# Kernel tuning notes

Measured on AMD Instinct MI355X. Metric: run time of the kernel, lower is better.

Reference implementation:

```python
import jax, jax.numpy as jnp
import numpy as np

B, T, N, D = 256, 200, 8, 64
MODEL = N * D          # 512
FFN_H = 1024 * N // 4  # 2048
EPS = 1.1920929e-07    # torch.finfo(float32).eps (nn.RMSNorm default eps=None)


def setup_inputs() -> dict:
    key = jax.random.key(0)
    ks = jax.random.split(key, 9)
    def xavier(k, shape):
        fan_in, fan_out = shape[-2], shape[-1]
        lim = float(np.sqrt(6.0 / (fan_in + fan_out)))
        return jax.random.uniform(k, shape, jnp.float32, -lim, lim)
    q = jax.random.normal(ks[0], (B, N, D), jnp.float32)
    seq = jax.random.normal(ks[1], (B, T, MODEL), jnp.float32)
    seq_mask = jax.random.randint(ks[2], (B, T), 0, 2) > 0
    seq_mask = seq_mask.at[:, 0].set(True)  # ensure >=1 valid position per row
    return {
        "q": q,
        "seq": seq,
        "rms_w": jnp.ones((MODEL,), jnp.float32),
        "w1": xavier(ks[3], (MODEL, FFN_H)),
        "w2": xavier(ks[4], (MODEL, FFN_H)),
        "w3": xavier(ks[5], (FFN_H, MODEL)),
        "w_k": xavier(ks[6], (N, D, D)),
        "w_v": xavier(ks[7], (N, D, D)),
        "seq_mask": seq_mask,
    }


def reference(q, seq, rms_w, w1, w2, w3, w_k, w_v, seq_mask):
    # RMSNorm
    sn = seq * jax.lax.rsqrt(jnp.mean(seq * seq, axis=-1, keepdims=True) + EPS) * rms_w
    # SwiGLU FFN + residual (dropout=0 / eval)
    h = (jax.nn.silu(sn @ w1) * (sn @ w2)) @ w3 + seq  # (B,T,N*D)
    hh = h.reshape(B, T, N, D)
    keys = jnp.einsum('btnd,nde->bnte', hh, w_k)    # (B,N,T,D)
    values = jnp.einsum('btnd,nde->bnte', hh, w_v)  # (B,N,T,D)
    scale = D ** (-0.5)
    scores = jnp.einsum('bnd,bntd->bnt', q, keys) * scale  # single-query attention
    scores = jnp.where(seq_mask[:, None, :], scores, -jnp.inf)
    attn = jax.nn.softmax(scores, axis=-1)
    ctx = jnp.einsum('bnt,bntd->bnd', attn, values)
    return ctx + q
```

## Files before the change

### kernel.cpp

```cpp
#include <hip/hip_runtime.h>
#include <hip/hip_fp16.h>
#include <cstdint>
#include <cstddef>

typedef unsigned short u16t;
typedef __bf16 bf16x8 __attribute__((ext_vector_type(8)));
typedef float f32x4 __attribute__((ext_vector_type(4)));
typedef unsigned short u16x8 __attribute__((ext_vector_type(8)));

#define BT_ROWS 51200
#define MODEL 512
#define FFNH 2048

__device__ __forceinline__ float bf2f(u16t u) {
  union { unsigned int i; float f; } v; v.i = ((unsigned int)u) << 16; return v.f;
}
__device__ __forceinline__ u16t f2bf(float f) {
  union { float f; unsigned int i; } v; v.f = f;
  return (u16t)((v.i + 0x7fffu + ((v.i >> 16) & 1u)) >> 16);
}
__device__ __forceinline__ float ldf(const void* p, size_t i, int dt) {
  if (dt == 1) return ((const float*)p)[i];
  u16t u = ((const u16t*)p)[i];
  if (dt == 0) return bf2f(u);
  __half h; *(u16t*)&h = u; return __half2float(h);
}
__device__ __forceinline__ void stf(void* p, size_t i, int dt, float f) {
  if (dt == 1) { ((float*)p)[i] = f; }
  else if (dt == 0) { ((u16t*)p)[i] = f2bf(f); }
  else { __half h = __float2half(f); ((u16t*)p)[i] = *(u16t*)&h; }
}
__device__ __forceinline__ void gl2lds16(const void* g, void* l) {
  __builtin_amdgcn_global_load_lds((const __attribute__((address_space(1))) void*)g,
                                   (__attribute__((address_space(3))) void*)l, 16, 0, 0);
}

__global__ __launch_bounds__(256) void detect_dtype_k(const unsigned int* __restrict__ w1,
                                                      int* __restrict__ cnts) {
  int i = blockIdx.x * 256 + threadIdx.x;
  unsigned int w = w1[i];
  u16t lo = (u16t)(w & 0xffffu), hi = (u16t)(w >> 16);
  float flo = bf2f(lo);
  int a = (!(fabsf(flo) < 0.25f)) ? 1 : 0;
  __half hh; *(u16t*)&hh = hi; float fhi = __half2float(hh);
  int b = (fabsf(fhi) > 0.25f && fabsf(fhi) < 256.f) ? 1 : 0;
  unsigned long long ba = __ballot(a), bb = __ballot(b);
  if ((threadIdx.x & 63) == 0) {
    atomicAdd(&cnts[0], (int)__popcll(ba));
    atomicAdd(&cnts[1], (int)__popcll(bb));
  }
}
__global__ void detect_finalize_k(const int* __restrict__ cnts, int* __restrict__ dflag) {
  if (threadIdx.x == 0)
    dflag[0] = (cnts[0] > 4096) ? 1 : ((cnts[1] < 4096) ? 2 : 0);
}

__global__ __launch_bounds__(256) void detect_mask_k(const unsigned int* __restrict__ msk,
                                                     int* __restrict__ flag) {
  int i = blockIdx.x * 256 + threadIdx.x;
  if (i < 12800) {
    unsigned int v = msk[i];
    if (v > 1u) atomicOr(flag, 1);
  }
}

__global__ __launch_bounds__(256) void rmsnorm_k(const void* __restrict__ seq,
                                                 const void* __restrict__ w,
                                                 const int* __restrict__ dfp,
                                                 u16t* __restrict__ xn) {
  const int dt = dfp[0];
  int row = blockIdx.x * 4 + (threadIdx.x >> 6);
  int lane = threadIdx.x & 63;
  size_t base = (size_t)row * MODEL + lane * 8;
  float x[8]; float ss = 0.f;
  if (dt == 0) {
    u16x8 xv = *(const u16x8*)((const u16t*)seq + base);
#pragma unroll
    for (int j = 0; j < 8; j++) { x[j] = bf2f(xv[j]); ss += x[j] * x[j]; }
  } else if (dt == 1) {
    const f32x4* p = (const f32x4*)((const float*)seq + base);
    f32x4 va = p[0], vb = p[1];
#pragma unroll
    for (int j = 0; j < 4; j++) { x[j] = va[j]; x[4 + j] = vb[j]; }
#pragma unroll
    for (int j = 0; j < 8; j++) ss += x[j] * x[j];
  } else {
#pragma unroll
    for (int j = 0; j < 8; j++) { x[j] = ldf(seq, base + j, dt); ss += x[j] * x[j]; }
  }
#pragma unroll
  for (int o = 32; o; o >>= 1) ss += __shfl_xor(ss, o);
  float rstd = rsqrtf(ss * (1.f / 512.f) + 1.1920929e-07f);
  u16x8 ov;
#pragma unroll
  for (int j = 0; j < 8; j++) ov[j] = f2bf(x[j] * rstd * ldf(w, lane * 8 + j, dt));
  *(u16x8*)(xn + base) = ov;
}

__global__ __launch_bounds__(256) void transpose_k(const void* __restrict__ src,
                                                   u16t* __restrict__ dst,
                                                   const int* __restrict__ dfp,
                                                   int R, int C) {
  const int dt = dfp[0];
  __shared__ u16t tile[32][33];
  int x = threadIdx.x & 31, y = threadIdx.x >> 5;
  int c0 = blockIdx.x * 32, r0 = blockIdx.y * 32;
#pragma unroll
  for (int i = 0; i < 32; i += 8)
    tile[y + i][x] = f2bf(ldf(src, (size_t)(r0 + y + i) * C + c0 + x, dt));
  __syncthreads();
#pragma unroll
  for (int i = 0; i < 32; i += 8) dst[(size_t)(c0 + y + i) * R + r0 + x] = tile[x][y + i];
}


__global__ __launch_bounds__(256, 2) void ffn_gemm1(const u16t* __restrict__ Xn,
                                                    const u16t* __restrict__ W1t,
                                                    const u16t* __restrict__ W2t,
                                                    u16t* __restrict__ Act) {
  __shared__ u16t As[128 * 64];
  __shared__ u16t B1s[64 * 64];
  __shared__ u16t B2s[64 * 64];
  const int tid = threadIdx.x;
  const int lane = tid & 63;
  const int wave = tid >> 6;
  const int wr = wave >> 1, wc = wave & 1;
  const int quad = lane >> 4, l16 = lane & 15;
  const int nBase = blockIdx.x * 64;
  const int mBase = blockIdx.y * 128;
  const int wuBase = tid & ~63;

  f32x4 acc1[4][2], acc2[4][2];
  const f32x4 zf = {0.f, 0.f, 0.f, 0.f};
#pragma unroll
  for (int i = 0; i < 4; i++)
#pragma unroll
    for (int j = 0; j < 2; j++) { acc1[i][j] = zf; acc2[i][j] = zf; }

  for (int kt = 0; kt < MODEL; kt += 64) {
#pragma unroll
    for (int c = 0; c < 4; c++) {
      int chunk = c * 256 + tid;
      int r = chunk >> 3, k8 = (chunk & 7) ^ (r & 7);
      gl2lds16(Xn + (size_t)(mBase + r) * MODEL + kt + k8 * 8, As + (size_t)(c * 256 + wuBase) * 8);
    }
#pragma unroll
    for (int c = 0; c < 2; c++) {
      int chunk = c * 256 + tid;
      int r = chunk >> 3, k8 = (chunk & 7) ^ (r & 7);
      gl2lds16(W1t + (size_t)(nBase + r) * MODEL + kt + k8 * 8, B1s + (size_t)(c * 256 + wuBase) * 8);
      gl2lds16(W2t + (size_t)(nBase + r) * MODEL + kt + k8 * 8, B2s + (size_t)(c * 256 + wuBase) * 8);
    }
    __syncthreads();
#pragma unroll
    for (int ks = 0; ks < 64; ks += 32) {
      bf16x8 a[4], b1[2], b2[2];
      const int sw = (ks >> 3) + quad;
#pragma unroll
      for (int mi = 0; mi < 4; mi++) {
        int row = wr * 64 + mi * 16 + l16;
        a[mi] = *(const bf16x8*)(As + row * 64 + ((sw ^ (row & 7)) << 3));
      }
#pragma unroll
      for (int ni = 0; ni < 2; ni++) {
        int row = wc * 32 + ni * 16 + l16;
        b1[ni] = *(const bf16x8*)(B1s + row * 64 + ((sw ^ (row & 7)) << 3));
        b2[ni] = *(const bf16x8*)(B2s + row * 64 + ((sw ^ (row & 7)) << 3));
      }
#pragma unroll
      for (int mi = 0; mi < 4; mi++)
#pragma unroll
        for (int ni = 0; ni < 2; ni++) {
          acc1[mi][ni] = __builtin_amdgcn_mfma_f32_16x16x32_bf16(a[mi], b1[ni], acc1[mi][ni], 0, 0, 0);
          acc2[mi][ni] = __builtin_amdgcn_mfma_f32_16x16x32_bf16(a[mi], b2[ni], acc2[mi][ni], 0, 0, 0);
        }
    }
    __syncthreads();
  }
#pragma unroll
  for (int mi = 0; mi < 4; mi++)
#pragma unroll
    for (int ni = 0; ni < 2; ni++)
#pragma unroll
      for (int r = 0; r < 4; r++) {
        int row = mBase + wr * 64 + mi * 16 + quad * 4 + r;
        int col = nBase + wc * 32 + ni * 16 + l16;
        float g1 = acc1[mi][ni][r], g2 = acc2[mi][ni][r];
        float sl = g1 / (1.f + __expf(-g1));
        Act[(size_t)row * FFNH + col] = f2bf(sl * g2);
      }
}

__global__ __launch_bounds__(256, 2) void ffn_gemm2(const u16t* __restrict__ Act,
                                                    const u16t* __restrict__ W3t,
                                                    const void* __restrict__ Seq,
                                                    const int* __restrict__ dfp,
                                                    u16t* __restrict__ H, int rowOff) {
  __shared__ u16t As[128 * 64];
  __shared__ u16t Bs[128 * 64];
  const int dt = dfp[0];
  const int tid = threadIdx.x;
  const int lane = tid & 63;
  const int wave = tid >> 6;
  const int wr = wave >> 1, wc = wave & 1;
  const int quad = lane >> 4, l16 = lane & 15;
  const int nBase = blockIdx.x * 128;
  const int mBase = blockIdx.y * 128;
  const int wuBase = tid & ~63;

  f32x4 acc[4][4];
  const f32x4 zf = {0.f, 0.f, 0.f, 0.f};
#pragma unroll
  for (int i = 0; i < 4; i++)
#pragma unroll
    for (int j = 0; j < 4; j++) acc[i][j] = zf;

  for (int kt = 0; kt < FFNH; kt += 64) {
#pragma unroll
    for (int c = 0; c < 4; c++) {
      int chunk = c * 256 + tid;
      int r = chunk >> 3, k8 = (chunk & 7) ^ (r & 7);
      gl2lds16(Act + (size_t)(mBase + r) * FFNH + kt + k8 * 8, As + (size_t)(c * 256 + wuBase) * 8);
      gl2lds16(W3t + (size_t)(nBase + r) * FFNH + kt + k8 * 8, Bs + (size_t)(c * 256 + wuBase) * 8);
    }
    __syncthreads();
#pragma unroll
    for (int ks = 0; ks < 64; ks += 32) {
      bf16x8 a[4], b[4];
      const int sw = (ks >> 3) + quad;
#pragma unroll
      for (int mi = 0; mi < 4; mi++) {
        int row = wr * 64 + mi * 16 + l16;
        a[mi] = *(const bf16x8*)(As + row * 64 + ((sw ^ (row & 7)) << 3));
      }
#pragma unroll
      for (int ni = 0; ni < 4; ni++) {
        int row = wc * 64 + ni * 16 + l16;
        b[ni] = *(const bf16x8*)(Bs + row * 64 + ((sw ^ (row & 7)) << 3));
      }
#pragma unroll
      for (int mi = 0; mi < 4; mi++)
#pragma unroll
        for (int ni = 0; ni < 4; ni++)
          acc[mi][ni] = __builtin_amdgcn_mfma_f32_16x16x32_bf16(a[mi], b[ni], acc[mi][ni], 0, 0, 0);
    }
    __syncthreads();
  }
#pragma unroll
  for (int mi = 0; mi < 4; mi++)
#pragma unroll
    for (int ni = 0; ni < 4; ni++)
#pragma unroll
      for (int r = 0; r < 4; r++) {
        int grow = rowOff + mBase + wr * 64 + mi * 16 + quad * 4 + r;
        int col = nBase + wc * 64 + ni * 16 + l16;
        float v = acc[mi][ni][r] + ldf(Seq, (size_t)grow * MODEL + col, dt);
        H[(size_t)grow * MODEL + col] = f2bf(v);
      }
}

__global__ __launch_bounds__(256) void attn_k(const u16t* __restrict__ H,
                                              const void* __restrict__ q,
                                              const void* __restrict__ wk,
                                              const void* __restrict__ wv,
                                              const int* __restrict__ mask,
                                              const int* __restrict__ mflagp,
                                              const int* __restrict__ dfp,
                                              void* __restrict__ out) {
  const int b = blockIdx.x >> 3;
  const int n = blockIdx.x & 7;
  const int tid = threadIdx.x;
  const int w = tid >> 6;
  const int lane = tid & 63;
  const int T = 200;
  const int HS = 66;
  const int dt = dfp[0];
  const int mflag = mflagp[0];

  __shared__ u16t hbuf[200 * HS];
  __shared__ float qk[64];
  __shared__ float sc[200];
  __shared__ float part[256];
  __shared__ float red[8];
  __shared__ float ctx[64];

  for (int chunk = tid; chunk < 1600; chunk += 256) {
    int r = chunk >> 3, c = (chunk & 7) << 3;
    u16x8 v = *(const u16x8*)(H + (size_t)(b * 200 + r) * MODEL + n * 64 + c);
#pragma unroll
    for (int j = 0; j < 8; j++) hbuf[r * HS + c + j] = v[j];
  }

  {
    int d = tid >> 2, sub = tid & 3;
    float s = 0.f;
    size_t wb = ((size_t)n * 64 + d) * 64 + sub * 16;
    size_t qb = (size_t)(b * 8 + n) * 64 + sub * 16;
#pragma unroll
    for (int i = 0; i < 16; i++) s += ldf(wk, wb + i, dt) * ldf(q, qb + i, dt);
    part[tid] = s;
  }
  __syncthreads();
  if (tid < 64) qk[tid] = part[tid * 4] + part[tid * 4 + 1] + part[tid * 4 + 2] + part[tid * 4 + 3];
  __syncthreads();

  float sv = -INFINITY;
  if (tid < T) {
    float s = 0.f;
#pragma unroll 16
    for (int d = 0; d < 64; d++) s += bf2f(hbuf[tid * HS + d]) * qk[d];
    int mv = mflag ? (int)((const unsigned char*)mask)[b * 200 + tid] : mask[b * 200 + tid];
    sv = mv ? s * 0.125f : -INFINITY;
  }

  float mx = sv;
#pragma unroll
  for (int o = 32; o; o >>= 1) mx = fmaxf(mx, __shfl_xor(mx, o));
  if (lane == 0) red[w] = mx;
  __syncthreads();
  float gmax = fmaxf(fmaxf(red[0], red[1]), fmaxf(red[2], red[3]));
  float e = 0.f;
  if (gmax == -INFINITY) {
    if (tid == 0) e = 1.f;
  } else if (tid < T) {
    e = __expf(sv - gmax);
  }
  float s = e;
#pragma unroll
  for (int o = 32; o; o >>= 1) s += __shfl_xor(s, o);
  if (lane == 0) red[4 + w] = s;
  __syncthreads();
  float inv = 1.f / (red[4] + red[5] + red[6] + red[7]);
  if (tid < T) sc[tid] = e * inv;
  __syncthreads();

  float a2 = 0.f;
  for (int t = w; t < T; t += 4) a2 += sc[t] * bf2f(hbuf[t * HS + lane]);
  part[tid] = a2;
  __syncthreads();
  if (tid < 64) ctx[tid] = part[tid] + part[64 + tid] + part[128 + tid] + part[192 + tid];
  __syncthreads();

  {
    int od = tid & 63;
    float s2 = 0.f;
#pragma unroll
    for (int i = 0; i < 16; i++) {
      int d = w * 16 + i;
      s2 += ctx[d] * ldf(wv, ((size_t)n * 64 + d) * 64 + od, dt);
    }
    part[tid] = s2;
  }
  __syncthreads();
  if (tid < 64) {
    size_t oi = (size_t)(b * 8 + n) * 64 + tid;
    stf(out, oi, dt,
        part[tid] + part[64 + tid] + part[128 + tid] + part[192 + tid] + ldf(q, oi, dt));
  }
}

extern "C" void kernel_launch(void* const* d_in, const int* in_sizes, int n_in,
                              void* d_out, int out_size, void* d_ws, size_t ws_size,
                              hipStream_t stream) {
  (void)in_sizes; (void)n_in; (void)out_size;
  const void* q   = d_in[0];
  const void* seq = d_in[1];
  const void* rw  = d_in[2];
  const void* w1  = d_in[3];
  const void* w2  = d_in[4];
  const void* w3  = d_in[5];
  const void* wk  = d_in[6];
  const void* wv  = d_in[7];
  const int*  msk = (const int*)d_in[8];

  char* ws = (char*)d_ws;
  size_t off = 0;
  auto alloc = [&](size_t b) { void* p = ws + off; off = (off + b + 255) & ~(size_t)255; return p; };
  int*  flags = (int*)alloc(512);
  int*  mflag = flags + 0;
  int*  cnts  = flags + 2;
  int*  dflag = flags + 4;
  u16t* Xn  = (u16t*)alloc((size_t)BT_ROWS * MODEL * 2);
  u16t* W1t = (u16t*)alloc((size_t)FFNH * MODEL * 2);
  u16t* W2t = (u16t*)alloc((size_t)FFNH * MODEL * 2);
  u16t* W3t = (u16t*)alloc((size_t)MODEL * FFNH * 2);
  size_t actBytes = (ws_size > off) ? (ws_size - off) : 0;
  long tpc = (long)(actBytes / ((size_t)128 * FFNH * 2));
  if (tpc < 1) tpc = 1;
  if (tpc > 100) tpc = 100;
  u16t* ActB = (u16t*)(ws + off);

  hipMemsetAsync(flags, 0, 512, stream);
  detect_dtype_k<<<dim3(1024), dim3(256), 0, stream>>>((const unsigned int*)w1, cnts);
  detect_finalize_k<<<dim3(1), dim3(64), 0, stream>>>(cnts, dflag);
  detect_mask_k<<<dim3(50), dim3(256), 0, stream>>>((const unsigned int*)msk, mflag);

  rmsnorm_k<<<dim3(BT_ROWS / 4), dim3(256), 0, stream>>>(seq, rw, dflag, Xn);
  transpose_k<<<dim3(FFNH / 32, MODEL / 32), dim3(256), 0, stream>>>(w1, W1t, dflag, MODEL, FFNH);
  transpose_k<<<dim3(FFNH / 32, MODEL / 32), dim3(256), 0, stream>>>(w2, W2t, dflag, MODEL, FFNH);
  transpose_k<<<dim3(MODEL / 32, FFNH / 32), dim3(256), 0, stream>>>(w3, W3t, dflag, FFNH, MODEL);

  for (int t0 = 0; t0 < 400; t0 += (int)tpc) {
    int tiles = (400 - t0 < (int)tpc) ? (400 - t0) : (int)tpc;
    int rows0 = t0 * 128;
    ffn_gemm1<<<dim3(FFNH / 64, tiles), dim3(256), 0, stream>>>(
        Xn + (size_t)rows0 * MODEL, W1t, W2t, ActB);
    ffn_gemm2<<<dim3(MODEL / 128, tiles), dim3(256), 0, stream>>>(
        ActB, W3t, seq, dflag, Xn, rows0);
  }
  attn_k<<<dim3(2048), dim3(256), 0, stream>>>(Xn, q, wk, wv, msk, mflag, dflag, d_out);
}
```

Baseline: 787.7 us.

## Shrink dtype detection to one block, raise occupancy bounds, enlarge GEMM chunking

Dtype detection now runs as a single block that samples 16K words with an in-block reduction, which removes the finalize kernel and the global atomics. The thresholds are scaled down to match the smaller sample. The mask check uses a wave ballot so only one atomic is issued per wave. Both FFN GEMMs get launch_bounds min-blocks raised from 2 to 4, which pushes the compiler toward fewer registers per thread and may cause spills. The cap on row tiles per chunk rises from 100 to 200, giving fewer and larger GEMM launches if the workspace is big enough.

Result: faster. 696.1 us (-11.6%).

```diff
diff --git a/kernel.cpp b/kernel.cpp
--- a/kernel.cpp
+++ b/kernel.cpp
@@ -36,32 +36,36 @@
 }
 
 __global__ __launch_bounds__(256) void detect_dtype_k(const unsigned int* __restrict__ w1,
-                                                      int* __restrict__ cnts) {
-  int i = blockIdx.x * 256 + threadIdx.x;
-  unsigned int w = w1[i];
-  u16t lo = (u16t)(w & 0xffffu), hi = (u16t)(w >> 16);
-  float flo = bf2f(lo);
-  int a = (!(fabsf(flo) < 0.25f)) ? 1 : 0;
-  __half hh; *(u16t*)&hh = hi; float fhi = __half2float(hh);
-  int b = (fabsf(fhi) > 0.25f && fabsf(fhi) < 256.f) ? 1 : 0;
-  unsigned long long ba = __ballot(a), bb = __ballot(b);
-  if ((threadIdx.x & 63) == 0) {
-    atomicAdd(&cnts[0], (int)__popcll(ba));
-    atomicAdd(&cnts[1], (int)__popcll(bb));
-  }
-}
-__global__ void detect_finalize_k(const int* __restrict__ cnts, int* __restrict__ dflag) {
-  if (threadIdx.x == 0)
-    dflag[0] = (cnts[0] > 4096) ? 1 : ((cnts[1] < 4096) ? 2 : 0);
+                                                      int* __restrict__ dflag) {
+  __shared__ int sh[8];
+  int a = 0, bc = 0;
+  for (int it = 0; it < 64; it++) {
+    unsigned int w = w1[it * 256 + threadIdx.x];
+    u16t lo = (u16t)(w & 0xffffu), hi = (u16t)(w >> 16);
+    float flo = bf2f(lo);
+    a += (!(fabsf(flo) < 0.25f)) ? 1 : 0;
+    __half hh; *(u16t*)&hh = hi; float fhi = __half2float(hh);
+    bc += (fabsf(fhi) > 0.25f && fabsf(fhi) < 256.f) ? 1 : 0;
+  }
+#pragma unroll
+  for (int o = 32; o; o >>= 1) { a += __shfl_xor(a, o); bc += __shfl_xor(bc, o); }
+  int w = threadIdx.x >> 6;
+  if ((threadIdx.x & 63) == 0) { sh[w] = a; sh[4 + w] = bc; }
+  __syncthreads();
+  if (threadIdx.x == 0) {
+    int A = sh[0] + sh[1] + sh[2] + sh[3];
+    int B = sh[4] + sh[5] + sh[6] + sh[7];
+    dflag[0] = (A > 256) ? 1 : ((B < 256) ? 2 : 0);
+  }
 }
 
 __global__ __launch_bounds__(256) void detect_mask_k(const unsigned int* __restrict__ msk,
                                                      int* __restrict__ flag) {
   int i = blockIdx.x * 256 + threadIdx.x;
-  if (i < 12800) {
-    unsigned int v = msk[i];
-    if (v > 1u) atomicOr(flag, 1);
-  }
+  int bad = 0;
+  if (i < 12800) bad = (msk[i] > 1u) ? 1 : 0;
+  unsigned long long bl = __ballot(bad);
+  if ((threadIdx.x & 63) == 0 && bl) atomicOr(flag, 1);
 }
 
 __global__ __launch_bounds__(256) void rmsnorm_k(const void* __restrict__ seq,
@@ -114,7 +118,7 @@
 }
 
 
-__global__ __launch_bounds__(256, 2) void ffn_gemm1(const u16t* __restrict__ Xn,
+__global__ __launch_bounds__(256, 4) void ffn_gemm1(const u16t* __restrict__ Xn,
                                                     const u16t* __restrict__ W1t,
                                                     const u16t* __restrict__ W2t,
                                                     u16t* __restrict__ Act) {
@@ -191,7 +195,7 @@
       }
 }
 
-__global__ __launch_bounds__(256, 2) void ffn_gemm2(const u16t* __restrict__ Act,
+__global__ __launch_bounds__(256, 4) void ffn_gemm2(const u16t* __restrict__ Act,
                                                     const u16t* __restrict__ W3t,
                                                     const void* __restrict__ Seq,
                                                     const int* __restrict__ dfp,
@@ -378,7 +382,6 @@
   auto alloc = [&](size_t b) { void* p = ws + off; off = (off + b + 255) & ~(size_t)255; return p; };
   int*  flags = (int*)alloc(512);
   int*  mflag = flags + 0;
-  int*  cnts  = flags + 2;
   int*  dflag = flags + 4;
   u16t* Xn  = (u16t*)alloc((size_t)BT_ROWS * MODEL * 2);
   u16t* W1t = (u16t*)alloc((size_t)FFNH * MODEL * 2);
@@ -387,12 +390,11 @@
   size_t actBytes = (ws_size > off) ? (ws_size - off) : 0;
   long tpc = (long)(actBytes / ((size_t)128 * FFNH * 2));
   if (tpc < 1) tpc = 1;
-  if (tpc > 100) tpc = 100;
+  if (tpc > 200) tpc = 200;
   u16t* ActB = (u16t*)(ws + off);
 
   hipMemsetAsync(flags, 0, 512, stream);
-  detect_dtype_k<<<dim3(1024), dim3(256), 0, stream>>>((const unsigned int*)w1, cnts);
-  detect_finalize_k<<<dim3(1), dim3(64), 0, stream>>>(cnts, dflag);
+  detect_dtype_k<<<dim3(1), dim3(256), 0, stream>>>((const unsigned int*)w1, dflag);
   detect_mask_k<<<dim3(50), dim3(256), 0, stream>>>((const unsigned int*)msk, mflag);
 
   rmsnorm_k<<<dim3(BT_ROWS / 4), dim3(256), 0, stream>>>(seq, rw, dflag, Xn);
```
